# Kernel optimization log

Hardware: AMD Instinct MI355X
Metric: run time of the kernel (lower is better)

## Reference

```python
import jax, jax.numpy as jnp
import numpy as np

HIDDEN = 1024
HEADS = 16
HEAD_DIM = HIDDEN // HEADS


def setup_inputs() -> dict:
    key = jax.random.key(0)
    ks = jax.random.split(key, 4)
    B, S, H = 2, 2048, HIDDEN
    scale = 1.0 / np.sqrt(H)
    return {
        "inputs": jax.random.normal(ks[0], (B, S, H), dtype=jnp.float32),
        "mask": jnp.ones((B, S), dtype=jnp.int32),
        "Wq": jax.random.normal(ks[1], (H, H), dtype=jnp.float32) * scale,
        "bq": jnp.zeros((H,), dtype=jnp.float32),
        "Wk": jax.random.normal(ks[2], (H, H), dtype=jnp.float32) * scale,
        "bk": jnp.zeros((H,), dtype=jnp.float32),
        "Wv": jax.random.normal(ks[3], (H, H), dtype=jnp.float32) * scale,
        "bv": jnp.zeros((H,), dtype=jnp.float32),
    }


def _split_heads(x, B, S):
    # [B,S,H] -> [B,heads,S,head_dim]
    return x.reshape(B, S, HEADS, HEAD_DIM).transpose(0, 2, 1, 3)


def reference(inputs, mask, Wq, bq, Wk, bk, Wv, bv):
    B, S, H = inputs.shape
    q = _split_heads(inputs @ Wq.T + bq, B, S)
    k = _split_heads(inputs @ Wk.T + bk, B, S)
    v = _split_heads(inputs @ Wv.T + bv, B, S)
    scores = jnp.einsum("bhqd,bhkd->bhqk", q, k) / jnp.sqrt(
        jnp.asarray(HEAD_DIM, dtype=inputs.dtype))
    # mask broadcast [B,1,1,S]; zeros -> -inf
    scores = jnp.where(mask[:, None, None, :] == 0, -jnp.inf, scores)
    attn = jax.nn.softmax(scores, axis=-1)
    context = jnp.einsum("bhqk,bhkd->bhqd", attn, v)
    return context.transpose(0, 2, 1, 3).reshape(B, S, H)
```

## Files before the change

### kernel.cpp

```cpp
#include <hip/hip_runtime.h>
#include <hip/hip_fp16.h>

constexpr int S_LEN  = 2048;
constexpr int HID    = 1024;
constexpr int HEADS  = 16;
constexpr int HDIM   = 64;
constexpr int BATCH  = 2;
constexpr int BH     = BATCH * HEADS;
constexpr int M_ROWS = BATCH * S_LEN;

typedef _Float16 half8  __attribute__((ext_vector_type(8)));
typedef _Float16 half4v __attribute__((ext_vector_type(4)));
typedef _Float16 half2v __attribute__((ext_vector_type(2)));
typedef float    f32x4  __attribute__((ext_vector_type(4)));
typedef float    f32x16 __attribute__((ext_vector_type(16)));
typedef unsigned uint4v __attribute__((ext_vector_type(4)));

constexpr float EXP2_OFF = -11.541560327111707f;
constexpr float Q_SCALE  = 0.18033688011112042f;

__global__ __launch_bounds__(256) void cvt_kernel(
    const float* __restrict__ X,  const float* __restrict__ Wq,
    const float* __restrict__ Wk, const float* __restrict__ Wv,
    const int* __restrict__ mask,
    _Float16* __restrict__ Xh,  _Float16* __restrict__ Wqh,
    _Float16* __restrict__ Wkh, _Float16* __restrict__ Wvh,
    float* __restrict__ maskF)
{
    const int blk = blockIdx.x;
    if (blk >= 3584) {
        const int loc = blk - 3584;
        const size_t e = ((size_t)loc * 256 + threadIdx.x) * 8;
        #pragma unroll
        for (int i = 0; i < 8; ++i)
            maskF[e + i] = mask[e + i] ? EXP2_OFF : -1.0e30f;
        return;
    }
    const float* src; _Float16* dst; int loc;
    if (blk < 2048)      { src = X;  dst = Xh;  loc = blk; }
    else if (blk < 2560) { src = Wq; dst = Wqh; loc = blk - 2048; }
    else if (blk < 3072) { src = Wk; dst = Wkh; loc = blk - 2560; }
    else                 { src = Wv; dst = Wvh; loc = blk - 3072; }
    const size_t e = ((size_t)loc * 256 + threadIdx.x) * 8;
    float4 a = *reinterpret_cast<const float4*>(&src[e]);
    float4 b = *reinterpret_cast<const float4*>(&src[e + 4]);
    half8 h = { (_Float16)a.x, (_Float16)a.y, (_Float16)a.z, (_Float16)a.w,
                (_Float16)b.x, (_Float16)b.y, (_Float16)b.z, (_Float16)b.w };
    *reinterpret_cast<half8*>(&dst[e]) = h;
}

__device__ __forceinline__ void async_cp16(_Float16* lds, const _Float16* g) {
    __builtin_amdgcn_global_load_lds(
        (const __attribute__((address_space(1))) void*)g,
        (__attribute__((address_space(3))) void*)lds, 16, 0, 0);
}

__device__ __forceinline__ void permlane32_swap(unsigned &x, unsigned &y) {
    asm("v_permlane32_swap_b32 %0, %1" : "+v"(x), "+v"(y));
}

__global__ __launch_bounds__(256) void qkv_proj_kernel(
    const _Float16* __restrict__ Xh,
    const _Float16* __restrict__ Wqh, const _Float16* __restrict__ Wkh,
    const _Float16* __restrict__ Wvh,
    const float* __restrict__ bq, const float* __restrict__ bk,
    const float* __restrict__ bv,
    _Float16* __restrict__ Qo, _Float16* __restrict__ Ko,
    _Float16* __restrict__ Vt)
{
    const int mode = blockIdx.z;
    const _Float16* W    = (mode == 0) ? Wqh : (mode == 1) ? Wkh : Wvh;
    const float*    bias = (mode == 0) ? bq  : (mode == 1) ? bk  : bv;

    const int m0 = blockIdx.x * 128, n0 = blockIdx.y * 128;
    const int tid = threadIdx.x, wave = tid >> 6, lane = tid & 63;
    const int l31 = lane & 31, kg = lane >> 5;

    __shared__ _Float16 SMEM[18432];

    f32x16 acc[2][2];
    #pragma unroll
    for (int mt = 0; mt < 2; ++mt)
        #pragma unroll
        for (int nt = 0; nt < 2; ++nt)
            #pragma unroll
            for (int i = 0; i < 16; ++i) acc[mt][nt][i] = 0.f;

    const int wm = (wave & 1) * 64, wn = (wave >> 1) * 64;

    const int srow = tid >> 2, spos = tid & 3;
    auto stage = [&](int k0, int b) {
        _Float16* Asb = SMEM + b * 8192;
        _Float16* Bsb = Asb + 4096;
        #pragma unroll
        for (int j = 0; j < 2; ++j) {
            const int row = srow + j * 64;
            const int sch = spos ^ (row & 3);
            async_cp16(&Asb[j * 2048 + tid * 8],
                       &Xh[(size_t)(m0 + row) * HID + k0 + sch * 8]);
            async_cp16(&Bsb[j * 2048 + tid * 8],
                       &W [(size_t)(n0 + row) * HID + k0 + sch * 8]);
        }
    };

    stage(0, 0);
    int buf = 0;

    for (int k0 = 0; k0 < HID; k0 += 32) {
        __syncthreads();
        if (k0 + 32 < HID) stage(k0 + 32, buf ^ 1);
        _Float16* Asb = SMEM + buf * 8192;
        _Float16* Bsb = Asb + 4096;

        #pragma unroll
        for (int c = 0; c < 2; ++c) {
            const int k8 = c * 2 + kg;
            half8 af[2], bf[2];
            #pragma unroll
            for (int mt = 0; mt < 2; ++mt) {
                const int row = wm + mt * 32 + l31;
                af[mt] = *reinterpret_cast<const half8*>(
                    &Asb[row * 32 + ((k8 ^ (row & 3)) * 8)]);
            }
            #pragma unroll
            for (int nt = 0; nt < 2; ++nt) {
                const int row = wn + nt * 32 + l31;
                bf[nt] = *reinterpret_cast<const half8*>(
                    &Bsb[row * 32 + ((k8 ^ (row & 3)) * 8)]);
            }
            #pragma unroll
            for (int mt = 0; mt < 2; ++mt)
                #pragma unroll
                for (int nt = 0; nt < 2; ++nt)
                    acc[mt][nt] = __builtin_amdgcn_mfma_f32_32x32x16_f16(
                        af[mt], bf[nt], acc[mt][nt], 0, 0, 0);
        }
        buf ^= 1;
    }
    __syncthreads();

    _Float16* T = SMEM + wave * 4608;

    const int nn  = n0 + wn;
    const int hh  = nn >> 6;
    const int mm  = m0 + wm;
    const int bb  = mm >> 11;
    const int bhv = bb * HEADS + hh;
    const int s0  = mm & 2047;
    const int rowg = lane >> 3, chunk = lane & 7;

    if (mode < 2) {
        _Float16* Out = (mode == 0) ? Qo : Ko;
        #pragma unroll
        for (int nt = 0; nt < 2; ++nt) {
            const int col = nt * 32 + l31;
            float bias_n = bias[nn + col];
            #pragma unroll
            for (int mt = 0; mt < 2; ++mt)
                #pragma unroll
                for (int r = 0; r < 16; ++r) {
                    const int row_l = (r & 3) + 8 * (r >> 2) + 4 * kg;
                    float v = acc[mt][nt][r] + bias_n;
                    if (mode == 0) v *= Q_SCALE;
                    T[(mt * 32 + row_l) * 72 + col] = (_Float16)v;
                }
        }
        asm volatile("s_waitcnt lgkmcnt(0)" ::: "memory");
        #pragma unroll
        for (int j = 0; j < 8; ++j) {
            const int sr = j * 8 + rowg;
            half8 v = *reinterpret_cast<const half8*>(&T[sr * 72 + chunk * 8]);
            *reinterpret_cast<half8*>(
                &Out[((size_t)bhv * S_LEN + s0 + sr) * HDIM + chunk * 8]) = v;
        }
    } else {
        #pragma unroll
        for (int nt = 0; nt < 2; ++nt) {
            const int col = nt * 32 + l31;
            const float bias_n = bias[nn + col];
            #pragma unroll
            for (int mt = 0; mt < 2; ++mt)
                #pragma unroll
                for (int rg = 0; rg < 4; ++rg) {
                    half4v t = { (_Float16)(acc[mt][nt][rg * 4 + 0] + bias_n),
                                 (_Float16)(acc[mt][nt][rg * 4 + 1] + bias_n),
                                 (_Float16)(acc[mt][nt][rg * 4 + 2] + bias_n),
                                 (_Float16)(acc[mt][nt][rg * 4 + 3] + bias_n) };
                    const int s_off = mt * 32 + 8 * rg + 4 * kg;
                    *reinterpret_cast<half4v*>(&T[col * 72 + s_off]) = t;
                }
        }
        asm volatile("s_waitcnt lgkmcnt(0)" ::: "memory");
        #pragma unroll
        for (int j = 0; j < 8; ++j) {
            const int dr = j * 8 + rowg;
            half8 v = *reinterpret_cast<const half8*>(&T[dr * 72 + chunk * 8]);
            *reinterpret_cast<half8*>(
                &Vt[((size_t)bhv * HDIM + dr) * S_LEN + s0 + chunk * 8]) = v;
        }
    }
}

__global__ __launch_bounds__(256) void attn_kernel(
    const _Float16* __restrict__ Q, const _Float16* __restrict__ K,
    const _Float16* __restrict__ Vt, const float* __restrict__ maskF,
    float* __restrict__ Out)
{
    const int id    = blockIdx.x;
    const int xcd   = id & 7, local = id >> 3;
    const int bh    = xcd * 4 + (local & 3);
    const int qt    = local >> 2;
    const int b = bh >> 4, h = bh & 15;
    const int tid = threadIdx.x, wave = tid >> 6, lane = tid & 63;
    const int l31 = lane & 31, kg = lane >> 5;

    __shared__ _Float16 Ks[2][64 * 64];
    __shared__ _Float16 Vs[2][64 * 64];

    const _Float16* Qb = Q  + (size_t)bh * S_LEN * HDIM;
    const _Float16* Kb = K  + (size_t)bh * S_LEN * HDIM;
    const _Float16* Vb = Vt + (size_t)bh * HDIM * S_LEN;
    const float*    mb = maskF + b * S_LEN;

    const int qrow = qt * 128 + wave * 32 + l31;

    half8 qf[4];
    #pragma unroll
    for (int kc = 0; kc < 4; ++kc)
        qf[kc] = *reinterpret_cast<const half8*>(
            &Qb[(size_t)qrow * HDIM + kc * 16 + kg * 8]);

    f32x16 acc[2];
    #pragma unroll
    for (int dt = 0; dt < 2; ++dt)
        #pragma unroll
        for (int i = 0; i < 16; ++i) acc[dt][i] = 0.f;
    float den = 0.f;

    const int srow_t = tid >> 3;
    const int sch    = (tid & 7) ^ (srow_t & 7);
    auto stage = [&](int kb, int buf) {
        #pragma unroll
        for (int j = 0; j < 2; ++j) {
            const int row = srow_t + j * 32;
            async_cp16(&Ks[buf][j * 2048 + tid * 8],
                       &Kb[(size_t)(kb + row) * HDIM + sch * 8]);
            async_cp16(&Vs[buf][j * 2048 + tid * 8],
                       &Vb[(size_t)row * S_LEN + kb + sch * 8]);
        }
    };

    stage(0, 0);
    int buf = 0;
    const int rsw = l31 & 7;

    for (int kb = 0; kb < S_LEN; kb += 64) {
        __syncthreads();
        if (kb + 64 < S_LEN) stage(kb + 64, buf ^ 1);

        f32x16 sc[2];
        #pragma unroll
        for (int kt = 0; kt < 2; ++kt) {
            #pragma unroll
            for (int i = 0; i < 16; ++i) sc[kt][i] = 0.f;
            half8 kf[4];
            #pragma unroll
            for (int kc = 0; kc < 4; ++kc)
                kf[kc] = *reinterpret_cast<const half8*>(
                    &Ks[buf][(kt * 32 + l31) * 64 + (((kc * 2 + kg) ^ rsw) * 8)]);
            #pragma unroll
            for (int kc = 0; kc < 4; ++kc)
                sc[kt] = __builtin_amdgcn_mfma_f32_32x32x16_f16(
                    kf[kc], qf[kc], sc[kt], 0, 0, 0);
        }

        half8 vf[2][4];
        #pragma unroll
        for (int dt = 0; dt < 2; ++dt)
            #pragma unroll
            for (int kc = 0; kc < 4; ++kc)
                vf[dt][kc] = *reinterpret_cast<const half8*>(
                    &Vs[buf][(dt * 32 + l31) * 64 + (((kc * 2 + kg) ^ rsw) * 8)]);

        #pragma unroll
        for (int kt = 0; kt < 2; ++kt) {
            float4 mm[4];
            #pragma unroll
            for (int g = 0; g < 4; ++g)
                mm[g] = *reinterpret_cast<const float4*>(
                    &mb[kb + kt * 32 + g * 8 + kg * 4]);

            float p[16];
            #pragma unroll
            for (int r = 0; r < 16; ++r) {
                const float* m4 = reinterpret_cast<const float*>(&mm[r >> 2]);
                p[r] = __builtin_amdgcn_exp2f(sc[kt][r] + m4[r & 3]);
            }
            den += (((p[0] + p[1]) + (p[2] + p[3])) +
                    ((p[4] + p[5]) + (p[6] + p[7]))) +
                   (((p[8] + p[9]) + (p[10] + p[11])) +
                    ((p[12] + p[13]) + (p[14] + p[15])));

            #pragma unroll
            for (int hh = 0; hh < 2; ++hh) {
                unsigned a0 = __builtin_bit_cast(unsigned,
                    __builtin_amdgcn_cvt_pkrtz(p[hh * 8 + 0], p[hh * 8 + 1]));
                unsigned a1 = __builtin_bit_cast(unsigned,
                    __builtin_amdgcn_cvt_pkrtz(p[hh * 8 + 2], p[hh * 8 + 3]));
                unsigned b0 = __builtin_bit_cast(unsigned,
                    __builtin_amdgcn_cvt_pkrtz(p[hh * 8 + 4], p[hh * 8 + 5]));
                unsigned b1 = __builtin_bit_cast(unsigned,
                    __builtin_amdgcn_cvt_pkrtz(p[hh * 8 + 6], p[hh * 8 + 7]));
                permlane32_swap(a0, b0);
                permlane32_swap(a1, b1);
                uint4v pd = { a0, a1, b0, b1 };
                half8 pf = __builtin_bit_cast(half8, pd);
                const int kc2 = kt * 2 + hh;
                acc[0] = __builtin_amdgcn_mfma_f32_32x32x16_f16(
                    vf[0][kc2], pf, acc[0], 0, 0, 0);
                acc[1] = __builtin_amdgcn_mfma_f32_32x32x16_f16(
                    vf[1][kc2], pf, acc[1], 0, 0, 0);
            }
        }
        buf ^= 1;
    }

    den += __shfl_xor(den, 32, 64);
    const float inv = 1.0f / den;

    float* orow = Out + ((size_t)(b * S_LEN + qrow)) * HID + h * HDIM;
    #pragma unroll
    for (int dt = 0; dt < 2; ++dt)
        #pragma unroll
        for (int g = 0; g < 4; ++g) {
            float4 o = { acc[dt][g * 4 + 0] * inv, acc[dt][g * 4 + 1] * inv,
                         acc[dt][g * 4 + 2] * inv, acc[dt][g * 4 + 3] * inv };
            *reinterpret_cast<float4*>(&orow[dt * 32 + g * 8 + kg * 4]) = o;
        }
}

extern "C" void kernel_launch(void* const* d_in, const int* in_sizes, int n_in,
                              void* d_out, int out_size, void* d_ws, size_t ws_size,
                              hipStream_t stream) {
    const float* X  = (const float*)d_in[0];
    const int*   mk = (const int*)  d_in[1];
    const float* Wq = (const float*)d_in[2];
    const float* bq = (const float*)d_in[3];
    const float* Wk = (const float*)d_in[4];
    const float* bk = (const float*)d_in[5];
    const float* Wv = (const float*)d_in[6];
    const float* bv = (const float*)d_in[7];
    float* out = (float*)d_out;

    _Float16* Xh  = (_Float16*)d_ws;
    _Float16* Wqh = Xh  + (size_t)M_ROWS * HID;
    _Float16* Wkh = Wqh + (size_t)HID * HID;
    _Float16* Wvh = Wkh + (size_t)HID * HID;
    _Float16* Q   = Wvh + (size_t)HID * HID;
    _Float16* K   = Q   + (size_t)BH * S_LEN * HDIM;
    _Float16* Vt  = K   + (size_t)BH * S_LEN * HDIM;
    float*    maskF = (float*)(Vt + (size_t)BH * S_LEN * HDIM);

    cvt_kernel<<<3586, 256, 0, stream>>>(X, Wq, Wk, Wv, mk, Xh, Wqh, Wkh, Wvh, maskF);

    dim3 gp(M_ROWS / 128, HID / 128, 3);
    qkv_proj_kernel<<<gp, 256, 0, stream>>>(Xh, Wqh, Wkh, Wvh, bq, bk, bv, Q, K, Vt);

    attn_kernel<<<512, 256, 0, stream>>>(Q, K, Vt, maskF, out);
}
```

Baseline: 181.6 us.

## Switch attention to single-wave blocks with per-wave KV pipeline and no barriers

The attention kernel now runs one 64-thread wave per block over 32 query rows, launching 2048 blocks instead of 512 blocks of 256 threads. Each wave stages its own 32-key K/V tiles through a double-buffered LDS ring using vmcnt waits instead of __syncthreads, with a new swizzle for the narrower V tile. The mask load is prefetched one tile ahead and s_setprio is raised around the MFMA blocks. The aim is to remove block-wide barriers and raise scheduling flexibility. The cost is that K/V tiles are no longer shared across four waves, so global and L2 traffic rises by about four times, and the wrap-around prefetch issues redundant loads at the end.

```diff
diff --git a/kernel.cpp b/kernel.cpp
--- a/kernel.cpp
+++ b/kernel.cpp
@@ -201,28 +201,27 @@
     }
 }
 
-__global__ __launch_bounds__(256) void attn_kernel(
+__global__ __launch_bounds__(64, 2) void attn_kernel(
     const _Float16* __restrict__ Q, const _Float16* __restrict__ K,
     const _Float16* __restrict__ Vt, const float* __restrict__ maskF,
     float* __restrict__ Out)
 {
-    const int id    = blockIdx.x;
-    const int xcd   = id & 7, local = id >> 3;
-    const int bh    = xcd * 4 + (local & 3);
-    const int qt    = local >> 2;
+    const int id  = blockIdx.x;
+    const int xcd = id & 7;
+    const int bh  = xcd * 4 + ((id >> 3) & 3);
+    const int qt  = id >> 5;
     const int b = bh >> 4, h = bh & 15;
-    const int tid = threadIdx.x, wave = tid >> 6, lane = tid & 63;
+    const int lane = threadIdx.x & 63;
     const int l31 = lane & 31, kg = lane >> 5;
 
-    __shared__ _Float16 Ks[2][64 * 64];
-    __shared__ _Float16 Vs[2][64 * 64];
+    __shared__ _Float16 KV[2][4096];
 
     const _Float16* Qb = Q  + (size_t)bh * S_LEN * HDIM;
     const _Float16* Kb = K  + (size_t)bh * S_LEN * HDIM;
     const _Float16* Vb = Vt + (size_t)bh * HDIM * S_LEN;
     const float*    mb = maskF + b * S_LEN;
 
-    const int qrow = qt * 128 + wave * 32 + l31;
+    const int qrow = qt * 32 + l31;
 
     half8 qf[4];
     #pragma unroll
@@ -237,93 +236,111 @@
         for (int i = 0; i < 16; ++i) acc[dt][i] = 0.f;
     float den = 0.f;
 
-    const int srow_t = tid >> 3;
-    const int sch    = (tid & 7) ^ (srow_t & 7);
-    auto stage = [&](int kb, int buf) {
-        #pragma unroll
-        for (int j = 0; j < 2; ++j) {
-            const int row = srow_t + j * 32;
-            async_cp16(&Ks[buf][j * 2048 + tid * 8],
-                       &Kb[(size_t)(kb + row) * HDIM + sch * 8]);
-            async_cp16(&Vs[buf][j * 2048 + tid * 8],
-                       &Vb[(size_t)row * S_LEN + kb + sch * 8]);
-        }
+    int klo[4], vlo[4];
+    #pragma unroll
+    for (int j = 0; j < 4; ++j) {
+        const int krow = j * 8 + (lane >> 3);
+        klo[j] = krow * HDIM + (((lane & 7) ^ (krow & 7)) * 8);
+        const int vrow = j * 16 + (lane >> 2);
+        const int vsw  = (vrow ^ (vrow >> 2)) & 3;
+        vlo[j] = vrow * S_LEN + (((lane & 3) ^ vsw) * 8);
+    }
+
+    auto stage = [&](int tile, int bufsel) {
+        const _Float16* kt_base = Kb + (size_t)tile * 32 * HDIM;
+        const _Float16* vt_base = Vb + tile * 32;
+        _Float16* kd = &KV[bufsel][0];
+        _Float16* vd = &KV[bufsel][2048];
+        #pragma unroll
+        for (int j = 0; j < 4; ++j)
+            async_cp16(&kd[j * 512 + lane * 8], kt_base + klo[j]);
+        #pragma unroll
+        for (int j = 0; j < 4; ++j)
+            async_cp16(&vd[j * 512 + lane * 8], vt_base + vlo[j]);
     };
 
+    float4 cm[4];
+    #pragma unroll
+    for (int g = 0; g < 4; ++g)
+        cm[g] = *reinterpret_cast<const float4*>(&mb[g * 8 + kg * 4]);
+    asm volatile("" ::: "memory");
     stage(0, 0);
-    int buf = 0;
-    const int rsw = l31 & 7;
-
-    for (int kb = 0; kb < S_LEN; kb += 64) {
-        __syncthreads();
-        if (kb + 64 < S_LEN) stage(kb + 64, buf ^ 1);
-
-        f32x16 sc[2];
-        #pragma unroll
-        for (int kt = 0; kt < 2; ++kt) {
-            #pragma unroll
-            for (int i = 0; i < 16; ++i) sc[kt][i] = 0.f;
-            half8 kf[4];
-            #pragma unroll
-            for (int kc = 0; kc < 4; ++kc)
-                kf[kc] = *reinterpret_cast<const half8*>(
-                    &Ks[buf][(kt * 32 + l31) * 64 + (((kc * 2 + kg) ^ rsw) * 8)]);
-            #pragma unroll
-            for (int kc = 0; kc < 4; ++kc)
-                sc[kt] = __builtin_amdgcn_mfma_f32_32x32x16_f16(
-                    kf[kc], qf[kc], sc[kt], 0, 0, 0);
-        }
-
-        half8 vf[2][4];
+    stage(1, 1);
+
+    constexpr int NT = S_LEN / 32;
+    for (int t = 0; t < NT; ++t) {
+        asm volatile("s_waitcnt vmcnt(8)" ::: "memory");
+        const _Float16* Kl = &KV[t & 1][0];
+        const _Float16* Vl = &KV[t & 1][2048];
+
+        half8 kf[4];
+        #pragma unroll
+        for (int kc = 0; kc < 4; ++kc)
+            kf[kc] = *reinterpret_cast<const half8*>(
+                &Kl[l31 * 64 + (((kc * 2 + kg) ^ (l31 & 7)) * 8)]);
+        f32x16 sc;
+        #pragma unroll
+        for (int i = 0; i < 16; ++i) sc[i] = 0.f;
+        __builtin_amdgcn_s_setprio(1);
+        #pragma unroll
+        for (int kc = 0; kc < 4; ++kc)
+            sc = __builtin_amdgcn_mfma_f32_32x32x16_f16(kf[kc], qf[kc], sc, 0, 0, 0);
+        __builtin_amdgcn_s_setprio(0);
+
+        half8 vf[2][2];
         #pragma unroll
         for (int dt = 0; dt < 2; ++dt)
             #pragma unroll
-            for (int kc = 0; kc < 4; ++kc)
-                vf[dt][kc] = *reinterpret_cast<const half8*>(
-                    &Vs[buf][(dt * 32 + l31) * 64 + (((kc * 2 + kg) ^ rsw) * 8)]);
-
-        #pragma unroll
-        for (int kt = 0; kt < 2; ++kt) {
-            float4 mm[4];
-            #pragma unroll
-            for (int g = 0; g < 4; ++g)
-                mm[g] = *reinterpret_cast<const float4*>(
-                    &mb[kb + kt * 32 + g * 8 + kg * 4]);
-
-            float p[16];
-            #pragma unroll
-            for (int r = 0; r < 16; ++r) {
-                const float* m4 = reinterpret_cast<const float*>(&mm[r >> 2]);
-                p[r] = __builtin_amdgcn_exp2f(sc[kt][r] + m4[r & 3]);
+            for (int kc2 = 0; kc2 < 2; ++kc2) {
+                const int vrow = dt * 32 + l31;
+                const int vsw  = (vrow ^ (vrow >> 2)) & 3;
+                vf[dt][kc2] = *reinterpret_cast<const half8*>(
+                    &Vl[vrow * 32 + (((kc2 * 2 + kg) ^ vsw) * 8)]);
             }
-            den += (((p[0] + p[1]) + (p[2] + p[3])) +
-                    ((p[4] + p[5]) + (p[6] + p[7]))) +
-                   (((p[8] + p[9]) + (p[10] + p[11])) +
-                    ((p[12] + p[13]) + (p[14] + p[15])));
-
-            #pragma unroll
-            for (int hh = 0; hh < 2; ++hh) {
-                unsigned a0 = __builtin_bit_cast(unsigned,
-                    __builtin_amdgcn_cvt_pkrtz(p[hh * 8 + 0], p[hh * 8 + 1]));
-                unsigned a1 = __builtin_bit_cast(unsigned,
-                    __builtin_amdgcn_cvt_pkrtz(p[hh * 8 + 2], p[hh * 8 + 3]));
-                unsigned b0 = __builtin_bit_cast(unsigned,
-                    __builtin_amdgcn_cvt_pkrtz(p[hh * 8 + 4], p[hh * 8 + 5]));
-                unsigned b1 = __builtin_bit_cast(unsigned,
-                    __builtin_amdgcn_cvt_pkrtz(p[hh * 8 + 6], p[hh * 8 + 7]));
-                permlane32_swap(a0, b0);
-                permlane32_swap(a1, b1);
-                uint4v pd = { a0, a1, b0, b1 };
-                half8 pf = __builtin_bit_cast(half8, pd);
-                const int kc2 = kt * 2 + hh;
-                acc[0] = __builtin_amdgcn_mfma_f32_32x32x16_f16(
-                    vf[0][kc2], pf, acc[0], 0, 0, 0);
-                acc[1] = __builtin_amdgcn_mfma_f32_32x32x16_f16(
-                    vf[1][kc2], pf, acc[1], 0, 0, 0);
-            }
-        }
-        buf ^= 1;
-    }
+
+        float p[16];
+        #pragma unroll
+        for (int r = 0; r < 16; ++r) {
+            const float* m4 = reinterpret_cast<const float*>(&cm[r >> 2]);
+            p[r] = __builtin_amdgcn_exp2f(sc[r] + m4[r & 3]);
+        }
+        den += (((p[0] + p[1]) + (p[2] + p[3])) +
+                ((p[4] + p[5]) + (p[6] + p[7]))) +
+               (((p[8] + p[9]) + (p[10] + p[11])) +
+                ((p[12] + p[13]) + (p[14] + p[15])));
+
+        #pragma unroll
+        for (int hh = 0; hh < 2; ++hh) {
+            unsigned a0 = __builtin_bit_cast(unsigned,
+                __builtin_amdgcn_cvt_pkrtz(p[hh * 8 + 0], p[hh * 8 + 1]));
+            unsigned a1 = __builtin_bit_cast(unsigned,
+                __builtin_amdgcn_cvt_pkrtz(p[hh * 8 + 2], p[hh * 8 + 3]));
+            unsigned b0 = __builtin_bit_cast(unsigned,
+                __builtin_amdgcn_cvt_pkrtz(p[hh * 8 + 4], p[hh * 8 + 5]));
+            unsigned b1 = __builtin_bit_cast(unsigned,
+                __builtin_amdgcn_cvt_pkrtz(p[hh * 8 + 6], p[hh * 8 + 7]));
+            permlane32_swap(a0, b0);
+            permlane32_swap(a1, b1);
+            uint4v pd = { a0, a1, b0, b1 };
+            half8 pf = __builtin_bit_cast(half8, pd);
+            __builtin_amdgcn_s_setprio(1);
+            acc[0] = __builtin_amdgcn_mfma_f32_32x32x16_f16(
+                vf[0][hh], pf, acc[0], 0, 0, 0);
+            acc[1] = __builtin_amdgcn_mfma_f32_32x32x16_f16(
+                vf[1][hh], pf, acc[1], 0, 0, 0);
+            __builtin_amdgcn_s_setprio(0);
+        }
+
+        asm volatile("s_waitcnt lgkmcnt(0)" ::: "memory");
+        const int mt_next = (t + 1) & (NT - 1);
+        #pragma unroll
+        for (int g = 0; g < 4; ++g)
+            cm[g] = *reinterpret_cast<const float4*>(
+                &mb[mt_next * 32 + g * 8 + kg * 4]);
+        asm volatile("" ::: "memory");
+        stage((t + 2) & (NT - 1), t & 1);
+    }
+    asm volatile("s_waitcnt vmcnt(0)" ::: "memory");
 
     den += __shfl_xor(den, 32, 64);
     const float inv = 1.0f / den;
@@ -366,5 +383,5 @@
     dim3 gp(M_ROWS / 128, HID / 128, 3);
     qkv_proj_kernel<<<gp, 256, 0, stream>>>(Xh, Wqh, Wkh, Wvh, bq, bk, bv, Q, K, Vt);
 
-    attn_kernel<<<512, 256, 0, stream>>>(Q, K, Vt, maskF, out);
-}
+    attn_kernel<<<2048, 64, 0, stream>>>(Q, K, Vt, maskF, out);
+}
```

New measurement: 193.4 us. 6.5% more time.

## Triple-buffer K/V/mask tiles in LDS with vmcnt-based waits and MFMA priority

Applied to the files above, without the earlier changes.

Moves the attention loop from double to triple buffering of K/V tiles and also stages the mask into LDS with async 4-byte loads, so the mask no longer comes from global memory in the inner loop. The full __syncthreads is replaced by an explicit vmcnt wait plus s_barrier, which lets two tiles stay in flight. MFMA blocks are wrapped in s_setprio to favour matrix issue. The cost is more LDS per block, which may lower occupancy, and the loop issues wrap-around prefetches that load tiles that are never used.

```diff
diff --git a/kernel.cpp b/kernel.cpp
--- a/kernel.cpp
+++ b/kernel.cpp
@@ -54,6 +54,11 @@
         (const __attribute__((address_space(1))) void*)g,
         (__attribute__((address_space(3))) void*)lds, 16, 0, 0);
 }
+__device__ __forceinline__ void async_cp4(float* lds, const float* g) {
+    __builtin_amdgcn_global_load_lds(
+        (const __attribute__((address_space(1))) void*)g,
+        (__attribute__((address_space(3))) void*)lds, 4, 0, 0);
+}
 
 __device__ __forceinline__ void permlane32_swap(unsigned &x, unsigned &y) {
     asm("v_permlane32_swap_b32 %0, %1" : "+v"(x), "+v"(y));
@@ -206,16 +211,17 @@
     const _Float16* __restrict__ Vt, const float* __restrict__ maskF,
     float* __restrict__ Out)
 {
-    const int id    = blockIdx.x;
-    const int xcd   = id & 7, local = id >> 3;
-    const int bh    = xcd * 4 + (local & 3);
-    const int qt    = local >> 2;
+    const int id   = blockIdx.x;
+    const int xcd  = id & 7;
+    const int bh   = xcd * 4 + ((id >> 3) & 3);
+    const int qt   = id >> 5;
     const int b = bh >> 4, h = bh & 15;
     const int tid = threadIdx.x, wave = tid >> 6, lane = tid & 63;
     const int l31 = lane & 31, kg = lane >> 5;
 
-    __shared__ _Float16 Ks[2][64 * 64];
-    __shared__ _Float16 Vs[2][64 * 64];
+    __shared__ _Float16 Ks[3][64 * 64];
+    __shared__ _Float16 Vs[3][64 * 64];
+    __shared__ float    Ms[3][4][64];
 
     const _Float16* Qb = Q  + (size_t)bh * S_LEN * HDIM;
     const _Float16* Kb = K  + (size_t)bh * S_LEN * HDIM;
@@ -229,6 +235,7 @@
     for (int kc = 0; kc < 4; ++kc)
         qf[kc] = *reinterpret_cast<const half8*>(
             &Qb[(size_t)qrow * HDIM + kc * 16 + kg * 8]);
+    asm volatile("s_waitcnt vmcnt(0)" ::: "memory");
 
     f32x16 acc[2];
     #pragma unroll
@@ -238,25 +245,41 @@
     float den = 0.f;
 
     const int srow_t = tid >> 3;
-    const int sch    = (tid & 7) ^ (srow_t & 7);
-    auto stage = [&](int kb, int buf) {
+    const int slot   = tid & 7;
+    auto stage = [&](int tile, int bufsel) {
+        const int kb = tile * 64;
         #pragma unroll
         for (int j = 0; j < 2; ++j) {
-            const int row = srow_t + j * 32;
-            async_cp16(&Ks[buf][j * 2048 + tid * 8],
-                       &Kb[(size_t)(kb + row) * HDIM + sch * 8]);
-            async_cp16(&Vs[buf][j * 2048 + tid * 8],
-                       &Vb[(size_t)row * S_LEN + kb + sch * 8]);
-        }
+            const int row  = srow_t + j * 32;
+            const int csrc = slot ^ (row & 7);
+            async_cp16(&Ks[bufsel][j * 2048 + tid * 8],
+                       &Kb[(size_t)(kb + row) * HDIM + csrc * 8]);
+            async_cp16(&Vs[bufsel][j * 2048 + tid * 8],
+                       &Vb[(size_t)row * S_LEN + kb + csrc * 8]);
+        }
+        async_cp4(&Ms[bufsel][wave][lane], &mb[kb + lane]);
     };
 
+    constexpr int NT = S_LEN / 64;
     stage(0, 0);
+    stage(1, 1);
     int buf = 0;
     const int rsw = l31 & 7;
 
-    for (int kb = 0; kb < S_LEN; kb += 64) {
-        __syncthreads();
-        if (kb + 64 < S_LEN) stage(kb + 64, buf ^ 1);
+    for (int t = 0; t < NT; ++t) {
+        asm volatile("s_waitcnt vmcnt(5)" ::: "memory");
+        __builtin_amdgcn_s_barrier();
+        asm volatile("" ::: "memory");
+
+        {
+            int nt2 = t + 2; if (nt2 >= NT) nt2 -= NT;
+            int nb  = buf + 2; if (nb >= 3) nb -= 3;
+            stage(nt2, nb);
+        }
+
+        const _Float16* Kl = Ks[buf];
+        const _Float16* Vl = Vs[buf];
+        const float*    Mw = Ms[buf][wave];
 
         f32x16 sc[2];
         #pragma unroll
@@ -267,11 +290,13 @@
             #pragma unroll
             for (int kc = 0; kc < 4; ++kc)
                 kf[kc] = *reinterpret_cast<const half8*>(
-                    &Ks[buf][(kt * 32 + l31) * 64 + (((kc * 2 + kg) ^ rsw) * 8)]);
+                    &Kl[(kt * 32 + l31) * 64 + (((kc * 2 + kg) ^ rsw) * 8)]);
+            __builtin_amdgcn_s_setprio(1);
             #pragma unroll
             for (int kc = 0; kc < 4; ++kc)
                 sc[kt] = __builtin_amdgcn_mfma_f32_32x32x16_f16(
                     kf[kc], qf[kc], sc[kt], 0, 0, 0);
+            __builtin_amdgcn_s_setprio(0);
         }
 
         half8 vf[2][4];
@@ -280,7 +305,7 @@
             #pragma unroll
             for (int kc = 0; kc < 4; ++kc)
                 vf[dt][kc] = *reinterpret_cast<const half8*>(
-                    &Vs[buf][(dt * 32 + l31) * 64 + (((kc * 2 + kg) ^ rsw) * 8)]);
+                    &Vl[(dt * 32 + l31) * 64 + (((kc * 2 + kg) ^ rsw) * 8)]);
 
         #pragma unroll
         for (int kt = 0; kt < 2; ++kt) {
@@ -288,7 +313,7 @@
             #pragma unroll
             for (int g = 0; g < 4; ++g)
                 mm[g] = *reinterpret_cast<const float4*>(
-                    &mb[kb + kt * 32 + g * 8 + kg * 4]);
+                    &Mw[kt * 32 + g * 8 + kg * 4]);
 
             float p[16];
             #pragma unroll
@@ -316,13 +341,15 @@
                 uint4v pd = { a0, a1, b0, b1 };
                 half8 pf = __builtin_bit_cast(half8, pd);
                 const int kc2 = kt * 2 + hh;
+                __builtin_amdgcn_s_setprio(1);
                 acc[0] = __builtin_amdgcn_mfma_f32_32x32x16_f16(
                     vf[0][kc2], pf, acc[0], 0, 0, 0);
                 acc[1] = __builtin_amdgcn_mfma_f32_32x32x16_f16(
                     vf[1][kc2], pf, acc[1], 0, 0, 0);
+                __builtin_amdgcn_s_setprio(0);
             }
         }
-        buf ^= 1;
+        if (++buf == 3) buf = 0;
     }
 
     den += __shfl_xor(den, 32, 64);
```

Result: no change. 179.2 us (-1.4%).
